# Kernel optimization log

Hardware: AMD Instinct MI355X
Metric: run time of the kernel (lower is better)

The kernel has to match this reference:

```python
import jax, jax.numpy as jnp
import numpy as np

NOISE_STD = 0.001


def setup_inputs() -> dict:
    key = jax.random.key(0)
    k1, k2, k3, k4 = jax.random.split(key, 4)
    B, T, NIN, NREC = 64, 2048, 64, 1024
    x = jax.random.normal(k1, (B, T, NIN), dtype=jnp.float32)
    W_ih = jax.random.normal(k2, (NREC, NIN), dtype=jnp.float32) / np.sqrt(NIN)
    W_hh = jax.random.normal(k3, (NREC, NREC), dtype=jnp.float32) / np.sqrt(NREC)
    noise = jax.random.normal(k4, (T, NREC), dtype=jnp.float32)
    return {"x": x, "W_ih": W_ih, "W_hh": W_hh, "noise": noise}


def reference(x, W_ih, W_hh, noise):
    # x: [B, T, n_in] -> scan over time (strict sequential dependency)
    B = x.shape[0]
    NREC = W_hh.shape[0]
    x_t = jnp.transpose(x, (1, 0, 2))            # [T, B, n_in]
    xproj = jnp.einsum('tbi,ri->tbr', x_t, W_ih)  # hoist input GEMM out of scan
    noise_scaled = noise * NOISE_STD              # [T, NREC], broadcast over batch
    h0 = jnp.zeros((B, NREC), dtype=x.dtype)

    def step(h_prev, inp):
        xp, n_t = inp
        h = xp + jnp.tanh(h_prev) @ W_hh.T + n_t[None, :]
        return h, h[-1]  # original appends h_t[-1] (last batch element)

    h_last, outs = jax.lax.scan(step, h0, (xproj, noise_scaled))
    output = outs.T  # stack -> [T, NREC], transpose(0,1) -> [NREC, T]
    return output, h_last
```

## Files before the change

### kernel.cpp

```cpp
#include <hip/hip_runtime.h>


#define TT    2048
#define BB    64
#define NIN   64
#define NRECN 1024
#define KTOT  1088
#define NGRP  8
#define WPGRP 16
#define NWG   128
#define NOISE_STD 0.001f

typedef __attribute__((ext_vector_type(8))) _Float16 half8;
typedef __attribute__((ext_vector_type(4))) float f32x4;
typedef __attribute__((ext_vector_type(2))) unsigned int u32x2;

__device__ __forceinline__ void st_d2_sc1(void* p, u32x2 w) {
  asm volatile("global_store_dwordx2 %0, %1, off sc1" :: "v"(p), "v"(w) : "memory");
}
__device__ __forceinline__ unsigned pk2h(float a, float b) {
  unsigned short ua = __builtin_bit_cast(unsigned short, (_Float16)a);
  unsigned short ub = __builtin_bit_cast(unsigned short, (_Float16)b);
  return (unsigned)ua | ((unsigned)ub << 16);
}
__device__ __forceinline__ void split8h(const f32x4& v0, const f32x4& v1,
                                        half8& hh, half8& hl) {
  #pragma unroll
  for (int j = 0; j < 4; ++j) {
    _Float16 h = (_Float16)v0[j];
    hh[j] = h; hl[j] = (_Float16)(v0[j] - (float)h);
  }
  #pragma unroll
  for (int j = 0; j < 4; ++j) {
    _Float16 h = (_Float16)v1[j];
    hh[4 + j] = h; hl[4 + j] = (_Float16)(v1[j] - (float)h);
  }
}

#define LDA16(V, P, OFF) \
  asm volatile("global_load_dwordx4 %0, %1, off offset:%c2" \
               : "=&v"(V) : "v"(P), "n"(OFF))
#define WAITV(N) asm volatile("s_waitcnt vmcnt(" #N ")" ::: "memory")

#define MFMA16 __builtin_amdgcn_mfma_f32_16x16x32_f16

#define ACHUNK(c) {                                            \
    half8 b0 = *(const half8*)(whp0 + (c) * 2048);             \
    half8 b1 = *(const half8*)(whp1 + (c) * 2048);             \
    if ((c) & 1) {                                             \
      Q0 = MFMA16(b0, A[c], Q0, 0, 0, 0);                      \
      Q1 = MFMA16(b1, A[c], Q1, 0, 0, 0);                      \
    } else {                                                   \
      P0 = MFMA16(b0, A[c], P0, 0, 0, 0);                      \
      P1 = MFMA16(b1, A[c], P1, 0, 0, 0);                      \
    } }

__global__ __launch_bounds__(128, 1) void rnn_scan_kernel(
    const float* __restrict__ x, const float* __restrict__ W_ih,
    const float* __restrict__ W_hh, const float* __restrict__ noise,
    float* __restrict__ out, int* __restrict__ flags,
    _Float16* __restrict__ th)
{
  extern __shared__ _Float16 smem[];

  const int wg = blockIdx.x, grp = wg & 7, gidx = wg >> 3;
  const int tid = threadIdx.x, lane = tid & 63, wv = tid >> 6;
  const int l15 = lane & 15, g4 = lane >> 4;

  for (int idx = tid; idx < 64 * KTOT; idx += 128) {
    int nr = idx / KTOT, k = idx - nr * KTOT;
    int ng = gidx * 64 + nr;
    float v = (k < NRECN) ? W_hh[(size_t)ng * NRECN + k]
                          : W_ih[(size_t)ng * NIN + (k - NRECN)];
    smem[(k >> 3) * 512 + nr * 8 + (k & 7)] = (_Float16)v;
  }
  __syncthreads();

  int* ctr = flags + grp * 16;
  const _Float16* whp0 = smem + g4 * 512 + (wv * 32 + l15) * 8;
  const _Float16* whp1 = whp0 + 128;
  _Float16* thg = th + grp * (2 * 8 * 1024);
  const int b_eff = grp * 8 + (l15 & 7);
  const float* xrow = x + (size_t)b_eff * TT * NIN;
  const int cB = gidx * 64 + wv * 32 + g4 * 4;

  for (int t = 0; t < TT; ++t) {
    const float* xp = xrow + (size_t)t * NIN + g4 * 8;
    f32x4 v0 = *(const f32x4*)xp,        v1 = *(const f32x4*)(xp + 4);
    f32x4 v2 = *(const f32x4*)(xp + 32), v3 = *(const f32x4*)(xp + 36);
    f32x4 nz0 = *(const f32x4*)(noise + (size_t)t * NRECN + cB);
    f32x4 nz1 = *(const f32x4*)(noise + (size_t)t * NRECN + cB + 16);
    #pragma unroll
    for (int r = 0; r < 4; ++r) { nz0[r] *= NOISE_STD; nz1[r] *= NOISE_STD; }

    f32x4 P0{0,0,0,0}, P1{0,0,0,0}, Q0{0,0,0,0}, Q1{0,0,0,0};
    {
      half8 xh, xl;
      split8h(v0, v1, xh, xl);
      half8 b0 = *(const half8*)(whp0 + 32 * 2048);
      half8 b1 = *(const half8*)(whp1 + 32 * 2048);
      P0 = MFMA16(b0, xh, P0, 0,0,0); P1 = MFMA16(b1, xh, P1, 0,0,0);
      Q0 = MFMA16(b0, xl, Q0, 0,0,0); Q1 = MFMA16(b1, xl, Q1, 0,0,0);
      split8h(v2, v3, xh, xl);
      b0 = *(const half8*)(whp0 + 33 * 2048);
      b1 = *(const half8*)(whp1 + 33 * 2048);
      P0 = MFMA16(b0, xh, P0, 0,0,0); P1 = MFMA16(b1, xh, P1, 0,0,0);
      Q0 = MFMA16(b0, xl, Q0, 0,0,0); Q1 = MFMA16(b1, xl, Q1, 0,0,0);
    }

    if (t > 0) {
      const int target = t * WPGRP;
      if (tid == 0) {
        while (__hip_atomic_load(ctr, __ATOMIC_RELAXED,
                                 __HIP_MEMORY_SCOPE_AGENT) < target) { }
      }
      if (wv == 0)
        __builtin_amdgcn_fence(__ATOMIC_ACQUIRE, "agent");
      __syncthreads();

      const _Float16* abase = thg + (t & 1) * 8192 + (l15 & 7) * 1024 + g4 * 8;
      half8 A[32];
      #pragma unroll
      for (int c = 0; c < 32; ++c) LDA16(A[c], abase, c * 64);
      WAITV(24); __builtin_amdgcn_sched_barrier(0);
      #pragma unroll
      for (int c = 0; c < 8; ++c) ACHUNK(c);
      WAITV(16); __builtin_amdgcn_sched_barrier(0);
      #pragma unroll
      for (int c = 8; c < 16; ++c) ACHUNK(c);
      WAITV(8);  __builtin_amdgcn_sched_barrier(0);
      #pragma unroll
      for (int c = 16; c < 24; ++c) ACHUNK(c);
      WAITV(0);  __builtin_amdgcn_sched_barrier(0);
      #pragma unroll
      for (int c = 24; c < 32; ++c) ACHUNK(c);
    }

    f32x4 h0 = (P0 + Q0) + nz0;
    f32x4 h1 = (P1 + Q1) + nz1;
    _Float16* ob = thg + ((t + 1) & 1) * 8192;
    float tv0[4], tv1[4];
    #pragma unroll
    for (int r = 0; r < 4; ++r) {
      tv0[r] = 1.f - 2.f / (__expf(2.f * h0[r]) + 1.f);
      tv1[r] = 1.f - 2.f / (__expf(2.f * h1[r]) + 1.f);
    }
    if (l15 < 8) {
      u32x2 w0, w1;
      w0[0] = pk2h(tv0[0], tv0[1]); w0[1] = pk2h(tv0[2], tv0[3]);
      w1[0] = pk2h(tv1[0], tv1[1]); w1[1] = pk2h(tv1[2], tv1[3]);
      st_d2_sc1(ob + l15 * 1024 + cB, w0);
      st_d2_sc1(ob + l15 * 1024 + cB + 16, w1);
    }
    __syncthreads();
    if (tid == 0)
      __hip_atomic_fetch_add(ctr, 1, __ATOMIC_RELAXED,
                             __HIP_MEMORY_SCOPE_AGENT);

    if (grp == 7 && l15 == 7) {
      #pragma unroll
      for (int r = 0; r < 4; ++r) {
        out[(size_t)(cB + r) * TT + t] = h0[r];
        out[(size_t)(cB + 16 + r) * TT + t] = h1[r];
      }
    }
    if (t == TT - 1 && l15 < 8) {
      const int br = grp * 8 + l15;
      *(f32x4*)(out + (size_t)NRECN * TT + (size_t)br * NRECN + cB) = h0;
      *(f32x4*)(out + (size_t)NRECN * TT + (size_t)br * NRECN + cB + 16) = h1;
    }
  }
}

extern "C" void kernel_launch(void* const* d_in, const int* in_sizes, int n_in,
                              void* d_out, int out_size, void* d_ws, size_t ws_size,
                              hipStream_t stream) {
  const float* x     = (const float*)d_in[0];
  const float* W_ih  = (const float*)d_in[1];
  const float* W_hh  = (const float*)d_in[2];
  const float* noise = (const float*)d_in[3];
  float* out = (float*)d_out;

  char* ws = (char*)d_ws;
  int* flags = (int*)ws;
  _Float16* th = (_Float16*)(ws + 4096);

  (void)hipMemsetAsync(flags, 0, 4096, stream);

  const size_t lds_bytes = (size_t)136 * 64 * 8 * sizeof(_Float16);
  (void)hipFuncSetAttribute((const void*)rnn_scan_kernel,
                            hipFuncAttributeMaxDynamicSharedMemorySize,
                            (int)lds_bytes);

  rnn_scan_kernel<<<dim3(NWG), dim3(128), lds_bytes, stream>>>(
      x, W_ih, W_hh, noise, out, flags, th);
}
```

Measured before the change: 10.79 ms.

## Keep half of W_hh in registers, sync per wave, drop x hi/lo split

The even K-chunks of W_hh and all of W_ih are now held in VGPRs, and only the odd K-chunks stay in LDS, which cuts LDS reads per step. The block-wide __syncthreads barriers are replaced by per-wave spinning on the counter, with a target of 32 arrivals per step, and a per-wave counter increment after a vmcnt wait. The x input projection now uses a single fp16 conversion instead of the hi/lo split, halving those MFMAs but lowering input precision. The x and noise loads are issued early through inline asm so they overlap the wait. The risks are high register pressure from 36 half8 registers and possible precision loss on the input term.

```diff
diff --git a/kernel.cpp b/kernel.cpp
--- a/kernel.cpp
+++ b/kernel.cpp
@@ -5,7 +5,6 @@
 #define BB    64
 #define NIN   64
 #define NRECN 1024
-#define KTOT  1088
 #define NGRP  8
 #define WPGRP 16
 #define NWG   128
@@ -23,37 +22,19 @@
   unsigned short ub = __builtin_bit_cast(unsigned short, (_Float16)b);
   return (unsigned)ua | ((unsigned)ub << 16);
 }
-__device__ __forceinline__ void split8h(const f32x4& v0, const f32x4& v1,
-                                        half8& hh, half8& hl) {
+__device__ __forceinline__ half8 cvt8(const f32x4& a, const f32x4& b) {
+  half8 r;
   #pragma unroll
-  for (int j = 0; j < 4; ++j) {
-    _Float16 h = (_Float16)v0[j];
-    hh[j] = h; hl[j] = (_Float16)(v0[j] - (float)h);
-  }
-  #pragma unroll
-  for (int j = 0; j < 4; ++j) {
-    _Float16 h = (_Float16)v1[j];
-    hh[4 + j] = h; hl[4 + j] = (_Float16)(v1[j] - (float)h);
-  }
+  for (int j = 0; j < 4; ++j) { r[j] = (_Float16)a[j]; r[4+j] = (_Float16)b[j]; }
+  return r;
 }
 
 #define LDA16(V, P, OFF) \
   asm volatile("global_load_dwordx4 %0, %1, off offset:%c2" \
                : "=&v"(V) : "v"(P), "n"(OFF))
 #define WAITV(N) asm volatile("s_waitcnt vmcnt(" #N ")" ::: "memory")
-
+#define SB0 __builtin_amdgcn_sched_barrier(0)
 #define MFMA16 __builtin_amdgcn_mfma_f32_16x16x32_f16
-
-#define ACHUNK(c) {                                            \
-    half8 b0 = *(const half8*)(whp0 + (c) * 2048);             \
-    half8 b1 = *(const half8*)(whp1 + (c) * 2048);             \
-    if ((c) & 1) {                                             \
-      Q0 = MFMA16(b0, A[c], Q0, 0, 0, 0);                      \
-      Q1 = MFMA16(b1, A[c], Q1, 0, 0, 0);                      \
-    } else {                                                   \
-      P0 = MFMA16(b0, A[c], P0, 0, 0, 0);                      \
-      P1 = MFMA16(b1, A[c], P1, 0, 0, 0);                      \
-    } }
 
 __global__ __launch_bounds__(128, 1) void rnn_scan_kernel(
     const float* __restrict__ x, const float* __restrict__ W_ih,
@@ -67,77 +48,107 @@
   const int tid = threadIdx.x, lane = tid & 63, wv = tid >> 6;
   const int l15 = lane & 15, g4 = lane >> 4;
 
-  for (int idx = tid; idx < 64 * KTOT; idx += 128) {
-    int nr = idx / KTOT, k = idx - nr * KTOT;
-    int ng = gidx * 64 + nr;
-    float v = (k < NRECN) ? W_hh[(size_t)ng * NRECN + k]
-                          : W_ih[(size_t)ng * NIN + (k - NRECN)];
-    smem[(k >> 3) * 512 + nr * 8 + (k & 7)] = (_Float16)v;
+  for (int idx = tid; idx < 64 * 512; idx += 128) {
+    int col = idx >> 9, kk = idx & 511;
+    int oc = kk >> 5, g = (kk >> 3) & 3, j = kk & 7;
+    int k = (2 * oc + 1) * 32 + g * 8 + j;
+    smem[(oc * 4 + g) * 512 + col * 8 + j] =
+        (_Float16)W_hh[(size_t)(gidx * 64 + col) * NRECN + k];
+  }
+
+  half8 Wr[36];
+  #pragma unroll
+  for (int e = 0; e < 16; ++e) {
+    const int k0 = (2 * e) * 32 + g4 * 8;
+    #pragma unroll
+    for (int tl = 0; tl < 2; ++tl) {
+      const int n = gidx * 64 + wv * 32 + tl * 16 + l15;
+      const float* wp = W_hh + (size_t)n * NRECN + k0;
+      Wr[e * 2 + tl] = cvt8(*(const f32x4*)wp, *(const f32x4*)(wp + 4));
+    }
+  }
+  #pragma unroll
+  for (int cx = 0; cx < 2; ++cx) {
+    const int k0 = cx * 32 + g4 * 8;
+    #pragma unroll
+    for (int tl = 0; tl < 2; ++tl) {
+      const int n = gidx * 64 + wv * 32 + tl * 16 + l15;
+      const float* wp = W_ih + (size_t)n * NIN + k0;
+      Wr[32 + cx * 2 + tl] = cvt8(*(const f32x4*)wp, *(const f32x4*)(wp + 4));
+    }
   }
   __syncthreads();
 
   int* ctr = flags + grp * 16;
-  const _Float16* whp0 = smem + g4 * 512 + (wv * 32 + l15) * 8;
-  const _Float16* whp1 = whp0 + 128;
   _Float16* thg = th + grp * (2 * 8 * 1024);
   const int b_eff = grp * 8 + (l15 & 7);
   const float* xrow = x + (size_t)b_eff * TT * NIN;
   const int cB = gidx * 64 + wv * 32 + g4 * 4;
+  const _Float16* wlp = smem + g4 * 512 + (wv * 32 + l15) * 8;
 
   for (int t = 0; t < TT; ++t) {
+    f32x4 v0, v1, v2, v3, n0, n1;
     const float* xp = xrow + (size_t)t * NIN + g4 * 8;
-    f32x4 v0 = *(const f32x4*)xp,        v1 = *(const f32x4*)(xp + 4);
-    f32x4 v2 = *(const f32x4*)(xp + 32), v3 = *(const f32x4*)(xp + 36);
-    f32x4 nz0 = *(const f32x4*)(noise + (size_t)t * NRECN + cB);
-    f32x4 nz1 = *(const f32x4*)(noise + (size_t)t * NRECN + cB + 16);
-    #pragma unroll
-    for (int r = 0; r < 4; ++r) { nz0[r] *= NOISE_STD; nz1[r] *= NOISE_STD; }
+    const float* np = noise + (size_t)t * NRECN + cB;
+    LDA16(v0, xp, 0);  LDA16(v1, xp, 16);
+    LDA16(v2, xp, 128); LDA16(v3, xp, 144);
+    LDA16(n0, np, 0);  LDA16(n1, np, 64);
 
     f32x4 P0{0,0,0,0}, P1{0,0,0,0}, Q0{0,0,0,0}, Q1{0,0,0,0};
-    {
-      half8 xh, xl;
-      split8h(v0, v1, xh, xl);
-      half8 b0 = *(const half8*)(whp0 + 32 * 2048);
-      half8 b1 = *(const half8*)(whp1 + 32 * 2048);
-      P0 = MFMA16(b0, xh, P0, 0,0,0); P1 = MFMA16(b1, xh, P1, 0,0,0);
-      Q0 = MFMA16(b0, xl, Q0, 0,0,0); Q1 = MFMA16(b1, xl, Q1, 0,0,0);
-      split8h(v2, v3, xh, xl);
-      b0 = *(const half8*)(whp0 + 33 * 2048);
-      b1 = *(const half8*)(whp1 + 33 * 2048);
-      P0 = MFMA16(b0, xh, P0, 0,0,0); P1 = MFMA16(b1, xh, P1, 0,0,0);
-      Q0 = MFMA16(b0, xl, Q0, 0,0,0); Q1 = MFMA16(b1, xl, Q1, 0,0,0);
-    }
 
     if (t > 0) {
-      const int target = t * WPGRP;
-      if (tid == 0) {
+      const int target = t * 32;
+      if (lane == 0) {
         while (__hip_atomic_load(ctr, __ATOMIC_RELAXED,
                                  __HIP_MEMORY_SCOPE_AGENT) < target) { }
       }
-      if (wv == 0)
-        __builtin_amdgcn_fence(__ATOMIC_ACQUIRE, "agent");
-      __syncthreads();
-
-      const _Float16* abase = thg + (t & 1) * 8192 + (l15 & 7) * 1024 + g4 * 8;
+      __builtin_amdgcn_fence(__ATOMIC_ACQUIRE, "agent");
+      asm volatile("s_waitcnt vmcnt(0) lgkmcnt(0)" ::: "memory");
+      SB0;
+
+      const _Float16* abase =
+          thg + (t & 1) * 8192 + (l15 & 7) * 1024 + g4 * 8;
       half8 A[32];
       #pragma unroll
       for (int c = 0; c < 32; ++c) LDA16(A[c], abase, c * 64);
-      WAITV(24); __builtin_amdgcn_sched_barrier(0);
+
       #pragma unroll
-      for (int c = 0; c < 8; ++c) ACHUNK(c);
-      WAITV(16); __builtin_amdgcn_sched_barrier(0);
-      #pragma unroll
-      for (int c = 8; c < 16; ++c) ACHUNK(c);
-      WAITV(8);  __builtin_amdgcn_sched_barrier(0);
-      #pragma unroll
-      for (int c = 16; c < 24; ++c) ACHUNK(c);
-      WAITV(0);  __builtin_amdgcn_sched_barrier(0);
-      #pragma unroll
-      for (int c = 24; c < 32; ++c) ACHUNK(c);
-    }
-
-    f32x4 h0 = (P0 + Q0) + nz0;
-    f32x4 h1 = (P1 + Q1) + nz1;
+      for (int blk = 0; blk < 4; ++blk) {
+        if (blk == 0) { WAITV(24); } else if (blk == 1) { WAITV(16); }
+        else if (blk == 2) { WAITV(8); } else { WAITV(0); }
+        SB0;
+        #pragma unroll
+        for (int c = blk * 8; c < blk * 8 + 8; ++c) {
+          if ((c & 1) == 0) {
+            P0 = MFMA16(Wr[(c >> 1) * 2 + 0], A[c], P0, 0, 0, 0);
+            P1 = MFMA16(Wr[(c >> 1) * 2 + 1], A[c], P1, 0, 0, 0);
+          } else {
+            const int oc = c >> 1;
+            half8 b0 = *(const half8*)(wlp + oc * 2048);
+            half8 b1 = *(const half8*)(wlp + oc * 2048 + 128);
+            Q0 = MFMA16(b0, A[c], Q0, 0, 0, 0);
+            Q1 = MFMA16(b1, A[c], Q1, 0, 0, 0);
+          }
+        }
+      }
+    } else {
+      WAITV(0);
+    }
+
+    {
+      half8 xh0 = cvt8(v0, v1), xh1 = cvt8(v2, v3);
+      P0 = MFMA16(Wr[32], xh0, P0, 0, 0, 0);
+      P1 = MFMA16(Wr[33], xh0, P1, 0, 0, 0);
+      P0 = MFMA16(Wr[34], xh1, P0, 0, 0, 0);
+      P1 = MFMA16(Wr[35], xh1, P1, 0, 0, 0);
+    }
+
+    f32x4 h0, h1;
+    #pragma unroll
+    for (int r = 0; r < 4; ++r) {
+      h0[r] = P0[r] + Q0[r] + n0[r] * NOISE_STD;
+      h1[r] = P1[r] + Q1[r] + n1[r] * NOISE_STD;
+    }
     _Float16* ob = thg + ((t + 1) & 1) * 8192;
     float tv0[4], tv1[4];
     #pragma unroll
@@ -152,8 +163,8 @@
       st_d2_sc1(ob + l15 * 1024 + cB, w0);
       st_d2_sc1(ob + l15 * 1024 + cB + 16, w1);
     }
-    __syncthreads();
-    if (tid == 0)
+    WAITV(0);
+    if (lane == 0)
       __hip_atomic_fetch_add(ctr, 1, __ATOMIC_RELAXED,
                              __HIP_MEMORY_SCOPE_AGENT);
 
@@ -187,7 +198,7 @@
 
   (void)hipMemsetAsync(flags, 0, 4096, stream);
 
-  const size_t lds_bytes = (size_t)136 * 64 * 8 * sizeof(_Float16);
+  const size_t lds_bytes = 64 * 512 * sizeof(_Float16);
   (void)hipFuncSetAttribute((const void*)rnn_scan_kernel,
                             hipFuncAttributeMaxDynamicSharedMemorySize,
                             (int)lds_bytes);
```

Result: slower. 14.86 ms (+37.7%).

## Prefetch next-step x/noise, drop fp16 split for input, stage A loads

Applied to the files above, without the earlier changes.

Loads the next timestep's x and noise values during the current step, so they no longer sit on the critical path after the barrier. The input projection now uses a single fp16 conversion instead of a hi/lo split, which halves the input MFMAs and moves them after the recurrent GEMM. The global loads of the h-state are also issued in staggered batches interleaved with MFMA chunks. The precision drop on x risks accuracy, and the added vmcnt(0) wait before the barrier could put prefetch latency on the critical path.

```diff
diff --git a/kernel.cpp b/kernel.cpp
--- a/kernel.cpp
+++ b/kernel.cpp
@@ -23,25 +23,18 @@
   unsigned short ub = __builtin_bit_cast(unsigned short, (_Float16)b);
   return (unsigned)ua | ((unsigned)ub << 16);
 }
-__device__ __forceinline__ void split8h(const f32x4& v0, const f32x4& v1,
-                                        half8& hh, half8& hl) {
+__device__ __forceinline__ half8 cvt8(const f32x4& a, const f32x4& b) {
+  half8 r;
   #pragma unroll
-  for (int j = 0; j < 4; ++j) {
-    _Float16 h = (_Float16)v0[j];
-    hh[j] = h; hl[j] = (_Float16)(v0[j] - (float)h);
-  }
-  #pragma unroll
-  for (int j = 0; j < 4; ++j) {
-    _Float16 h = (_Float16)v1[j];
-    hh[4 + j] = h; hl[4 + j] = (_Float16)(v1[j] - (float)h);
-  }
+  for (int j = 0; j < 4; ++j) { r[j] = (_Float16)a[j]; r[4+j] = (_Float16)b[j]; }
+  return r;
 }
 
 #define LDA16(V, P, OFF) \
   asm volatile("global_load_dwordx4 %0, %1, off offset:%c2" \
                : "=&v"(V) : "v"(P), "n"(OFF))
 #define WAITV(N) asm volatile("s_waitcnt vmcnt(" #N ")" ::: "memory")
-
+#define SB0 __builtin_amdgcn_sched_barrier(0)
 #define MFMA16 __builtin_amdgcn_mfma_f32_16x16x32_f16
 
 #define ACHUNK(c) {                                            \
@@ -84,29 +77,15 @@
   const float* xrow = x + (size_t)b_eff * TT * NIN;
   const int cB = gidx * 64 + wv * 32 + g4 * 4;
 
+  f32x4 xv0, xv1, xv2, xv3, nv0, nv1;
+  { const float* xp = xrow + g4 * 8;
+    xv0 = *(const f32x4*)xp;        xv1 = *(const f32x4*)(xp + 4);
+    xv2 = *(const f32x4*)(xp + 32); xv3 = *(const f32x4*)(xp + 36);
+    nv0 = *(const f32x4*)(noise + cB);
+    nv1 = *(const f32x4*)(noise + cB + 16); }
+
   for (int t = 0; t < TT; ++t) {
-    const float* xp = xrow + (size_t)t * NIN + g4 * 8;
-    f32x4 v0 = *(const f32x4*)xp,        v1 = *(const f32x4*)(xp + 4);
-    f32x4 v2 = *(const f32x4*)(xp + 32), v3 = *(const f32x4*)(xp + 36);
-    f32x4 nz0 = *(const f32x4*)(noise + (size_t)t * NRECN + cB);
-    f32x4 nz1 = *(const f32x4*)(noise + (size_t)t * NRECN + cB + 16);
-    #pragma unroll
-    for (int r = 0; r < 4; ++r) { nz0[r] *= NOISE_STD; nz1[r] *= NOISE_STD; }
-
     f32x4 P0{0,0,0,0}, P1{0,0,0,0}, Q0{0,0,0,0}, Q1{0,0,0,0};
-    {
-      half8 xh, xl;
-      split8h(v0, v1, xh, xl);
-      half8 b0 = *(const half8*)(whp0 + 32 * 2048);
-      half8 b1 = *(const half8*)(whp1 + 32 * 2048);
-      P0 = MFMA16(b0, xh, P0, 0,0,0); P1 = MFMA16(b1, xh, P1, 0,0,0);
-      Q0 = MFMA16(b0, xl, Q0, 0,0,0); Q1 = MFMA16(b1, xl, Q1, 0,0,0);
-      split8h(v2, v3, xh, xl);
-      b0 = *(const half8*)(whp0 + 33 * 2048);
-      b1 = *(const half8*)(whp1 + 33 * 2048);
-      P0 = MFMA16(b0, xh, P0, 0,0,0); P1 = MFMA16(b1, xh, P1, 0,0,0);
-      Q0 = MFMA16(b0, xl, Q0, 0,0,0); Q1 = MFMA16(b1, xl, Q1, 0,0,0);
-    }
 
     if (t > 0) {
       const int target = t * WPGRP;
@@ -118,26 +97,59 @@
         __builtin_amdgcn_fence(__ATOMIC_ACQUIRE, "agent");
       __syncthreads();
 
-      const _Float16* abase = thg + (t & 1) * 8192 + (l15 & 7) * 1024 + g4 * 8;
+      const _Float16* abase =
+          thg + (t & 1) * 8192 + (l15 & 7) * 1024 + g4 * 8;
       half8 A[32];
       #pragma unroll
-      for (int c = 0; c < 32; ++c) LDA16(A[c], abase, c * 64);
-      WAITV(24); __builtin_amdgcn_sched_barrier(0);
-      #pragma unroll
-      for (int c = 0; c < 8; ++c) ACHUNK(c);
-      WAITV(16); __builtin_amdgcn_sched_barrier(0);
+      for (int c = 0; c < 8; ++c)  LDA16(A[c], abase, c * 64);
+      #pragma unroll
+      for (int c = 8; c < 16; ++c) LDA16(A[c], abase, c * 64);
+      WAITV(8);  SB0;
+      #pragma unroll
+      for (int c = 16; c < 24; ++c) LDA16(A[c], abase, c * 64);
+      #pragma unroll
+      for (int c = 0; c < 8; ++c)  ACHUNK(c);
+      WAITV(8);  SB0;
+      #pragma unroll
+      for (int c = 24; c < 32; ++c) LDA16(A[c], abase, c * 64);
       #pragma unroll
       for (int c = 8; c < 16; ++c) ACHUNK(c);
-      WAITV(8);  __builtin_amdgcn_sched_barrier(0);
+      WAITV(8);  SB0;
       #pragma unroll
       for (int c = 16; c < 24; ++c) ACHUNK(c);
-      WAITV(0);  __builtin_amdgcn_sched_barrier(0);
+      WAITV(0);  SB0;
       #pragma unroll
       for (int c = 24; c < 32; ++c) ACHUNK(c);
     }
 
-    f32x4 h0 = (P0 + Q0) + nz0;
-    f32x4 h1 = (P1 + Q1) + nz1;
+    {
+      half8 xh0 = cvt8(xv0, xv1), xh1 = cvt8(xv2, xv3);
+      half8 b0 = *(const half8*)(whp0 + 32 * 2048);
+      half8 b1 = *(const half8*)(whp1 + 32 * 2048);
+      P0 = MFMA16(b0, xh0, P0, 0, 0, 0);
+      P1 = MFMA16(b1, xh0, P1, 0, 0, 0);
+      b0 = *(const half8*)(whp0 + 33 * 2048);
+      b1 = *(const half8*)(whp1 + 33 * 2048);
+      P0 = MFMA16(b0, xh1, P0, 0, 0, 0);
+      P1 = MFMA16(b1, xh1, P1, 0, 0, 0);
+    }
+
+    f32x4 y0, y1, y2, y3, m0, m1;
+    {
+      const int tt = (t + 1 < TT) ? t + 1 : t;
+      const float* xp = xrow + (size_t)tt * NIN + g4 * 8;
+      const float* np = noise + (size_t)tt * NRECN + cB;
+      LDA16(y0, xp, 0);   LDA16(y1, xp, 16);
+      LDA16(y2, xp, 128); LDA16(y3, xp, 144);
+      LDA16(m0, np, 0);   LDA16(m1, np, 64);
+    }
+
+    f32x4 h0, h1;
+    #pragma unroll
+    for (int r = 0; r < 4; ++r) {
+      h0[r] = P0[r] + Q0[r] + nv0[r] * NOISE_STD;
+      h1[r] = P1[r] + Q1[r] + nv1[r] * NOISE_STD;
+    }
     _Float16* ob = thg + ((t + 1) & 1) * 8192;
     float tv0[4], tv1[4];
     #pragma unroll
@@ -152,10 +164,13 @@
       st_d2_sc1(ob + l15 * 1024 + cB, w0);
       st_d2_sc1(ob + l15 * 1024 + cB + 16, w1);
     }
+    WAITV(0);
     __syncthreads();
     if (tid == 0)
       __hip_atomic_fetch_add(ctr, 1, __ATOMIC_RELAXED,
                              __HIP_MEMORY_SCOPE_AGENT);
+
+    xv0 = y0; xv1 = y1; xv2 = y2; xv3 = y3; nv0 = m0; nv1 = m1;
 
     if (grp == 7 && l15 == 7) {
       #pragma unroll
```

Measured after the change: 10.10 ms. -6.4%, faster.
